# Optimization experiments

Hardware: AMD Instinct MI355X
Metric: run time of the kernel (lower is better)

The kernel has to match this reference:

```python
import jax, jax.numpy as jnp
import numpy as np

N_NODES = 100000
N_EDGES = 3200000
N_GRAPHS = 1000
FEAT = 512
EMB = 7
N_CLASSES = 10


def gcn_conv(x, W, b, src, dst, n_nodes):
    # PyG GCNConv: add self-loops, symmetric normalization, aggregate src->dst.
    h = x @ W  # [N, emb] — transform first (emb is tiny)
    loops = jnp.arange(n_nodes, dtype=src.dtype)
    es = jnp.concatenate([src, loops])
    ed = jnp.concatenate([dst, loops])
    deg = jax.ops.segment_sum(jnp.ones_like(ed, dtype=h.dtype), ed, num_segments=n_nodes)
    dinv = jnp.where(deg > 0, jax.lax.rsqrt(deg), 0.0)
    norm = dinv[es] * dinv[ed]  # [E+N]
    msgs = h[es] * norm[:, None]
    out = jax.ops.segment_sum(msgs, ed, num_segments=n_nodes)
    return out + b


def setup_inputs() -> dict:
    key = jax.random.key(0)
    ks = jax.random.split(key, 8)
    x = jax.random.normal(ks[0], (N_NODES, FEAT), dtype=jnp.float32)
    edge_index = jax.random.randint(ks[1], (2, N_EDGES), 0, N_NODES, dtype=jnp.int64)
    batch_index = jnp.sort(jax.random.randint(ks[2], (N_NODES,), 0, N_GRAPHS, dtype=jnp.int64))
    s_in = 1.0 / np.sqrt(FEAT)
    s_h = 1.0 / np.sqrt(EMB)
    W_in = jax.random.uniform(ks[3], (FEAT, EMB), jnp.float32, -s_in, s_in)
    b_in = jnp.zeros((EMB,), jnp.float32)
    W_conv1 = jax.random.uniform(ks[4], (EMB, EMB), jnp.float32, -s_h, s_h)
    b_conv1 = jnp.zeros((EMB,), jnp.float32)
    W_out = jax.random.uniform(ks[5], (EMB, N_CLASSES), jnp.float32, -s_h, s_h)
    b_out = jax.random.uniform(ks[6], (N_CLASSES,), jnp.float32, -s_h, s_h)
    return {"x": x, "edge_index": edge_index, "batch_index": batch_index,
            "W_in": W_in, "b_in": b_in, "W_conv1": W_conv1, "b_conv1": b_conv1,
            "W_out": W_out, "b_out": b_out}


def reference(x, edge_index, batch_index, W_in, b_in, W_conv1, b_conv1, W_out, b_out):
    src, dst = edge_index[0], edge_index[1]
    out = jax.nn.relu(gcn_conv(x, W_in, b_in, src, dst, N_NODES))  # [N, 7]
    # final_conv_acts (computed by the original but NOT used in the returned logits)
    _final_conv_acts = jax.nn.relu(gcn_conv(out, W_conv1, b_conv1, src, dst, N_NODES))
    # global mean pool over batch_index (on `out`, matching the original forward)
    sums = jax.ops.segment_sum(out, batch_index, num_segments=N_GRAPHS)
    counts = jax.ops.segment_sum(jnp.ones((N_NODES,), out.dtype), batch_index, num_segments=N_GRAPHS)
    pooled = sums / jnp.maximum(counts, 1.0)[:, None]  # [G, 7]
    logits = pooled @ W_out + b_out  # [G, classes]
    return jax.nn.softmax(logits, axis=1)
```

## Files before the change

kernel.cpp:

```cpp
#include <hip/hip_runtime.h>

#define N_NODES   100000
#define N_EDGES   3200000
#define N_GRAPHS  1000
#define FEAT      512
#define EMB       7
#define HP        8
#define N_CLASSES 10

#define BSH       8
#define DMASK     255
#define NBUCK     391
#define TCOLS     392
#define NB_A      512
#define TILE_A    6250
#define NIT       25
#define SEGCAP    9216
#define GSPAN     16
#define MM_SB     295
#define MM_NC     96

__device__ __forceinline__ int load_idx(const void* p, long long i, int is32) {
    if (is32) return ((const int*)p)[i];
    return (int)((const long long*)p)[i];
}

__device__ int edge_is32(const void* p) {
    __shared__ int sflag;
    if (threadIdx.x == 0) sflag = 0;
    __syncthreads();
    const int* w = (const int*)p;
    int any = 0;
    for (int k = threadIdx.x; k < 2048; k += blockDim.x)
        if (w[2 * k + 1] != 0) any = 1;
    if (any) atomicOr(&sflag, 1);
    __syncthreads();
    return sflag;
}

__device__ int batch_is32(const void* p) {
    __shared__ int sflag;
    if (threadIdx.x == 0) sflag = 0;
    __syncthreads();
    const int* w = (const int*)p;
    int any = 0;
    for (int k = 1024 + threadIdx.x; k < 2048; k += blockDim.x)
        if (w[2 * k + 1] != 0) any = 1;
    if (any) atomicOr(&sflag, 1);
    __syncthreads();
    return sflag;
}

__device__ void mm_span(int nbase, const float* __restrict__ x,
                        const float* __restrict__ W, float* __restrict__ h) {
    int n = nbase + (int)threadIdx.x;
    if (n >= N_NODES) return;
    const float4* xr = (const float4*)(x + (size_t)n * FEAT);
    float acc[EMB];
#pragma unroll
    for (int j = 0; j < EMB; ++j) acc[j] = 0.0f;
#pragma unroll 4
    for (int k4 = 0; k4 < FEAT / 4; ++k4) {
        float4 v = xr[k4];
        const float* w = W + k4 * 4 * EMB;
#pragma unroll
        for (int j = 0; j < EMB; ++j) {
            float a = acc[j];
            a = fmaf(v.x, w[0 * EMB + j], a);
            a = fmaf(v.y, w[1 * EMB + j], a);
            a = fmaf(v.z, w[2 * EMB + j], a);
            a = fmaf(v.w, w[3 * EMB + j], a);
            acc[j] = a;
        }
    }
    float4* o = (float4*)(h + (size_t)n * HP);
    o[0] = make_float4(acc[0], acc[1], acc[2], acc[3]);
    o[1] = make_float4(acc[4], acc[5], acc[6], 0.0f);
}

__global__ void k_sortblk(const void* __restrict__ eidx, int* __restrict__ T,
                          int* __restrict__ gpk, const float* __restrict__ x,
                          const float* __restrict__ W, float* __restrict__ h) {
    if (blockIdx.x >= NB_A) { mm_span(((int)blockIdx.x - NB_A) * 256, x, W, h); return; }
    __shared__ int stage[TILE_A];
    __shared__ int bins[NBUCK];
    __shared__ int cur[NBUCK];
    __shared__ int pairv[256];
    __shared__ int wsum[4];
    int is32 = edge_is32(eidx);
    const int b = (int)blockIdx.x, t = (int)threadIdx.x;
    for (int k = t; k < NBUCK; k += 256) bins[k] = 0;
    __syncthreads();
    long long e0 = (long long)b * TILE_A;
    int pk[NIT], bk[NIT];
#pragma unroll
    for (int it = 0; it < NIT; ++it) {
        int i = it * 256 + t;
        if (i < TILE_A) {
            int src = load_idx(eidx, e0 + i, is32);
            int d   = load_idx(eidx, (long long)N_EDGES + e0 + i, is32);
            pk[it] = src | ((d & DMASK) << 17);
            bk[it] = d >> BSH;
            atomicAdd(&bins[bk[it]], 1);
        } else { pk[it] = 0; bk[it] = -1; }
    }
    __syncthreads();
    int c0 = (2 * t     < NBUCK) ? bins[2 * t]     : 0;
    int c1 = (2 * t + 1 < NBUCK) ? bins[2 * t + 1] : 0;
    int pr = c0 + c1;
    int inc = pr;
    for (int o = 1; o < 64; o <<= 1) {
        int u = __shfl_up(inc, o);
        if ((t & 63) >= o) inc += u;
    }
    if ((t & 63) == 63) wsum[t >> 6] = inc;
    pairv[t] = inc;
    __syncthreads();
    int add = 0, wv = t >> 6;
    if (wv >= 1) add += wsum[0];
    if (wv >= 2) add += wsum[1];
    if (wv >= 3) add += wsum[2];
    int excl = inc + add - pr;
    __syncthreads();
    if (2 * t     < NBUCK) { bins[2 * t]     = excl;      cur[2 * t]     = excl; }
    if (2 * t + 1 < NBUCK) { bins[2 * t + 1] = excl + c0; cur[2 * t + 1] = excl + c0; }
    __syncthreads();
    for (int k = t; k < NBUCK; k += 256)
        T[b * TCOLS + k] = b * TILE_A + bins[k];
    if (t == 0) T[b * TCOLS + NBUCK] = (b + 1) * TILE_A;
#pragma unroll
    for (int it = 0; it < NIT; ++it) {
        if (bk[it] >= 0) {
            int slot = atomicAdd(&cur[bk[it]], 1);
            stage[slot] = pk[it];
        }
    }
    __syncthreads();
    for (int i = t; i < TILE_A; i += 256)
        gpk[b * TILE_A + i] = stage[i];
}

__device__ int load_runs(const int* __restrict__ T, int k,
                         int* rstart, int* rst, int* wsum) {
    const int t = (int)threadIdx.x;
    int b0 = 2 * t, b1 = 2 * t + 1;
    int s0 = T[b0 * TCOLS + k], e0 = T[b0 * TCOLS + k + 1];
    int s1 = T[b1 * TCOLS + k], e1 = T[b1 * TCOLS + k + 1];
    rstart[b0] = s0; rstart[b1] = s1;
    int c0 = e0 - s0, c1 = e1 - s1;
    int pr = c0 + c1;
    int inc = pr;
    for (int o = 1; o < 64; o <<= 1) {
        int u = __shfl_up(inc, o);
        if ((t & 63) >= o) inc += u;
    }
    if ((t & 63) == 63) wsum[t >> 6] = inc;
    __syncthreads();
    int add = 0, wv = t >> 6;
    if (wv >= 1) add += wsum[0];
    if (wv >= 2) add += wsum[1];
    if (wv >= 3) add += wsum[2];
    int excl = inc + add - pr;
    rst[b0] = excl;
    rst[b1] = excl + c0;
    if (t == 255) rst[512] = excl + pr;
    __syncthreads();
    return rst[512];
}

__device__ __forceinline__ int run_of(const int* rst, int i) {
    int lo = 0, hi = 512;
    while (lo + 1 < hi) { int m = (lo + hi) >> 1; if (rst[m] <= i) lo = m; else hi = m; }
    return lo;
}

__global__ void k_nodecnt(const int* __restrict__ T, const int* __restrict__ gpk,
                          int* __restrict__ cnt, float* __restrict__ gsum,
                          const float* __restrict__ x, const float* __restrict__ W,
                          float* __restrict__ h) {
    if (blockIdx.x >= NBUCK) { mm_span((MM_SB + (int)blockIdx.x - NBUCK) * 256, x, W, h); return; }
    __shared__ int rstart[512], rst[513], wsum[4];
    __shared__ int bin[256];
    const int k = (int)blockIdx.x, t = (int)threadIdx.x;
    if (k < 32) {
        int idx = k * 256 + t;
        if (idx < N_GRAPHS * 8) gsum[idx] = 0.0f;
    }
    bin[t] = 0;
    int total = load_runs(T, k, rstart, rst, wsum);
    __syncthreads();
    int chunk = (total + 255) >> 8;
    int i0 = t * chunk;
    int i1 = i0 + chunk; if (i1 > total) i1 = total;
    if (i0 < total) {
        int cur = run_of(rst, i0);
        int nxt = rst[cur + 1];
        int addr = rstart[cur] + (i0 - rst[cur]);
        for (int i = i0; i < i1; ++i) {
            while (i >= nxt) { ++cur; addr = rstart[cur] + (i - rst[cur]); nxt = rst[cur + 1]; }
            int p = gpk[addr++];
            atomicAdd(&bin[(p >> 17) & DMASK], 1);
        }
    }
    __syncthreads();
    int node = (k << BSH) + t;
    if (node < N_NODES) cnt[node] = bin[t];
}

__global__ void k_ggather(const int* __restrict__ T, const int* __restrict__ gpk,
                          const int* __restrict__ cnt, const float* __restrict__ h,
                          const float* __restrict__ b_in, const void* __restrict__ batch,
                          float* __restrict__ gsum) {
    __shared__ int stage[SEGCAP];
    __shared__ int rstart[512], rst[513], wsum[4];
    __shared__ int bin[256], loff[256], curs[256], pairv[256];
    __shared__ float gsl[GSPAN][8];
    __shared__ int gmin_s;
    const int k = (int)blockIdx.x, t = (int)threadIdx.x;
    int bis32 = batch_is32(batch);
    if (t == 0) gmin_s = load_idx(batch, (long long)(k << BSH), bis32);
    if (t < GSPAN * 8) ((float*)gsl)[t] = 0.0f;
    int total = load_runs(T, k, rstart, rst, wsum);
    int len = (total > SEGCAP) ? SEGCAP : total;
    {
        int node = (k << BSH) + t;
        bin[t] = (node < N_NODES) ? cnt[node] : 0;
        curs[t] = 0;
    }
    __syncthreads();
    const int gmin = gmin_s;
    {
        int v = bin[t];
        int inc = v;
        for (int o = 1; o < 64; o <<= 1) {
            int u = __shfl_up(inc, o);
            if ((t & 63) >= o) inc += u;
        }
        pairv[t] = inc;
        __syncthreads();
        int add = 0, wv = t >> 6;
        if (wv >= 1) add += pairv[63];
        if (wv >= 2) add += pairv[127];
        if (wv >= 3) add += pairv[191];
        loff[t] = inc + add - v;
    }
    __syncthreads();
    int chunk = (len + 255) >> 8;
    int i0 = t * chunk;
    int i1 = i0 + chunk; if (i1 > len) i1 = len;
    if (i0 < len) {
        int cur = run_of(rst, i0);
        int nxt = rst[cur + 1];
        int addr = rstart[cur] + (i0 - rst[cur]);
        for (int i = i0; i < i1; ++i) {
            while (i >= nxt) { ++cur; addr = rstart[cur] + (i - rst[cur]); nxt = rst[cur + 1]; }
            int p = gpk[addr++];
            int dl = (p >> 17) & DMASK;
            int r = atomicAdd(&curs[dl], 1);
            stage[loff[dl] + r] = p & 0x1FFFF;
        }
    }
    __syncthreads();
    const float4* h4 = (const float4*)h;
    int q = t & 3;
#pragma unroll
    for (int g4 = 0; g4 < 4; ++g4) {
        int nl = (t >> 2) + g4 * 64;
        int node = (k << BSH) + nl;
        if (node < N_NODES) {
            int o = loff[nl], c = bin[nl];
            float acc[EMB];
#pragma unroll
            for (int j = 0; j < EMB; ++j) acc[j] = 0.0f;
            for (int kk = q; kk < c; kk += 4) {
                int s = stage[o + kk];
                float f = rsqrtf((float)cnt[s] + 1.0f);
                float4 a4 = h4[(size_t)s * 2];
                float4 c4 = h4[(size_t)s * 2 + 1];
                acc[0] = fmaf(a4.x, f, acc[0]); acc[1] = fmaf(a4.y, f, acc[1]);
                acc[2] = fmaf(a4.z, f, acc[2]); acc[3] = fmaf(a4.w, f, acc[3]);
                acc[4] = fmaf(c4.x, f, acc[4]); acc[5] = fmaf(c4.y, f, acc[5]);
                acc[6] = fmaf(c4.z, f, acc[6]);
            }
            float di = rsqrtf((float)c + 1.0f);
            if (q == 0) {
                float4 a4 = h4[(size_t)node * 2];
                float4 c4 = h4[(size_t)node * 2 + 1];
                acc[0] = fmaf(a4.x, di, acc[0]); acc[1] = fmaf(a4.y, di, acc[1]);
                acc[2] = fmaf(a4.z, di, acc[2]); acc[3] = fmaf(a4.w, di, acc[3]);
                acc[4] = fmaf(c4.x, di, acc[4]); acc[5] = fmaf(c4.y, di, acc[5]);
                acc[6] = fmaf(c4.z, di, acc[6]);
            }
#pragma unroll
            for (int j = 0; j < EMB; ++j) {
                acc[j] += __shfl_xor(acc[j], 1);
                acc[j] += __shfl_xor(acc[j], 2);
            }
            int j0 = 2 * q;
            float v0 = fmaxf(fmaf(di, acc[j0], b_in[j0]), 0.0f);
            float v1 = (j0 + 1 < EMB)
                     ? fmaxf(fmaf(di, acc[j0 + 1], b_in[j0 + 1]), 0.0f) : 0.0f;
            int g = load_idx(batch, node, bis32);
            int gi = g - gmin;
            if (gi < GSPAN) {
                atomicAdd(&gsl[gi][j0], v0);
                atomicAdd(&gsl[gi][j0 + 1], v1);
            } else {
                atomicAdd(&gsum[(size_t)g * 8 + j0], v0);
                atomicAdd(&gsum[(size_t)g * 8 + j0 + 1], v1);
            }
        }
    }
    __syncthreads();
    if (t < GSPAN * 8) {
        int r = t >> 3, c = t & 7;
        float v = gsl[r][c];
        int g = gmin + r;
        if (v != 0.0f && g < N_GRAPHS) atomicAdd(&gsum[(size_t)g * 8 + c], v);
    }
}

__global__ void k_final(const float* __restrict__ gsum, const void* __restrict__ batch,
                        const float* __restrict__ W_out, const float* __restrict__ b_out,
                        float* __restrict__ out) {
    int is32 = batch_is32(batch);
    int g = (int)blockIdx.x * 256 + (int)threadIdx.x;
    if (g >= N_GRAPHS) return;
    int n0, n1;
    {
        int lo = 0, hi = N_NODES;
        while (lo < hi) { int m = (lo + hi) >> 1; if (load_idx(batch, m, is32) < g) lo = m + 1; else hi = m; }
        n0 = lo;
        hi = N_NODES;
        while (lo < hi) { int m = (lo + hi) >> 1; if (load_idx(batch, m, is32) < g + 1) lo = m + 1; else hi = m; }
        n1 = lo;
    }
    float inv = 1.0f / fmaxf((float)(n1 - n0), 1.0f);
    float sums[EMB];
#pragma unroll
    for (int j = 0; j < EMB; ++j) sums[j] = gsum[(size_t)g * 8 + j] * inv;
    float logit[N_CLASSES];
    float mx = -1e30f;
#pragma unroll
    for (int c = 0; c < N_CLASSES; ++c) {
        float l = b_out[c];
#pragma unroll
        for (int j = 0; j < EMB; ++j)
            l = fmaf(sums[j], W_out[j * N_CLASSES + c], l);
        logit[c] = l;
        mx = fmaxf(mx, l);
    }
    float se = 0.0f;
#pragma unroll
    for (int c = 0; c < N_CLASSES; ++c) {
        logit[c] = expf(logit[c] - mx);
        se += logit[c];
    }
    float is = 1.0f / se;
#pragma unroll
    for (int c = 0; c < N_CLASSES; ++c)
        out[(size_t)g * N_CLASSES + c] = logit[c] * is;
}

extern "C" void kernel_launch(void* const* d_in, const int* in_sizes, int n_in,
                              void* d_out, int out_size, void* d_ws, size_t ws_size,
                              hipStream_t stream) {
    const float* x     = (const float*)d_in[0];
    const void*  eidx  = d_in[1];
    const void*  batch = d_in[2];
    const float* W_in  = (const float*)d_in[3];
    const float* b_in  = (const float*)d_in[4];
    const float* W_out = (const float*)d_in[7];
    const float* b_out = (const float*)d_in[8];
    float* out = (float*)d_out;

    int*   gpk  = (int*)d_ws;
    int*   T    = gpk + N_EDGES;
    int*   cnt  = T + NB_A * TCOLS;
    float* h    = (float*)(cnt + N_NODES);
    float* gsum = h + (size_t)N_NODES * HP;

    const int B = 256;
    k_sortblk<<<NB_A + MM_SB, B, 0, stream>>>(eidx, T, gpk, x, W_in, h);
    k_nodecnt<<<NBUCK + MM_NC, B, 0, stream>>>(T, gpk, cnt, gsum, x, W_in, h);
    k_ggather<<<NBUCK, B, 0, stream>>>(T, gpk, cnt, h, b_in, batch, gsum);
    k_final  <<<(N_GRAPHS + B - 1) / B, B, 0, stream>>>(gsum, batch, W_out, b_out, out);
}
```

Before: 157.8 us.

## Use 512-thread blocks and fold final softmax into last gather block

The count and gather kernels now run with 512 threads per block, so each thread loads one tile's run bounds instead of two and the scans widen to eight waves. The separate final kernel is removed: the last block to finish the gather, found through an atomic done counter with a threadfence, computes the pooled means and softmax. This saves one kernel launch and may raise per-block parallelism. In exchange, the final stage runs serially inside a single block. The mm_span calls inside the count kernel are reindexed with a 512-row stride, so there are now half as many of those blocks.

```diff
diff --git a/kernel.cpp b/kernel.cpp
--- a/kernel.cpp
+++ b/kernel.cpp
@@ -18,7 +18,7 @@
 #define SEGCAP    9216
 #define GSPAN     16
 #define MM_SB     295
-#define MM_NC     96
+#define MM_NC     48
 
 __device__ __forceinline__ int load_idx(const void* p, long long i, int is32) {
     if (is32) return ((const int*)p)[i];
@@ -140,56 +140,45 @@
         gpk[b * TILE_A + i] = stage[i];
 }
 
-__device__ int load_runs(const int* __restrict__ T, int k,
-                         int* rstart, int* rst, int* wsum) {
-    const int t = (int)threadIdx.x;
-    int b0 = 2 * t, b1 = 2 * t + 1;
-    int s0 = T[b0 * TCOLS + k], e0 = T[b0 * TCOLS + k + 1];
-    int s1 = T[b1 * TCOLS + k], e1 = T[b1 * TCOLS + k + 1];
-    rstart[b0] = s0; rstart[b1] = s1;
-    int c0 = e0 - s0, c1 = e1 - s1;
-    int pr = c0 + c1;
-    int inc = pr;
-    for (int o = 1; o < 64; o <<= 1) {
-        int u = __shfl_up(inc, o);
-        if ((t & 63) >= o) inc += u;
-    }
-    if ((t & 63) == 63) wsum[t >> 6] = inc;
-    __syncthreads();
-    int add = 0, wv = t >> 6;
-    if (wv >= 1) add += wsum[0];
-    if (wv >= 2) add += wsum[1];
-    if (wv >= 3) add += wsum[2];
-    int excl = inc + add - pr;
-    rst[b0] = excl;
-    rst[b1] = excl + c0;
-    if (t == 255) rst[512] = excl + pr;
-    __syncthreads();
-    return rst[512];
-}
-
 __device__ __forceinline__ int run_of(const int* rst, int i) {
     int lo = 0, hi = 512;
     while (lo + 1 < hi) { int m = (lo + hi) >> 1; if (rst[m] <= i) lo = m; else hi = m; }
     return lo;
 }
 
-__global__ void k_nodecnt(const int* __restrict__ T, const int* __restrict__ gpk,
-                          int* __restrict__ cnt, float* __restrict__ gsum,
-                          const float* __restrict__ x, const float* __restrict__ W,
-                          float* __restrict__ h) {
-    if (blockIdx.x >= NBUCK) { mm_span((MM_SB + (int)blockIdx.x - NBUCK) * 256, x, W, h); return; }
-    __shared__ int rstart[512], rst[513], wsum[4];
+__global__ void __launch_bounds__(512)
+k_nodecnt(const int* __restrict__ T, const int* __restrict__ gpk,
+          int* __restrict__ cnt, float* __restrict__ gsum, int* __restrict__ done,
+          const float* __restrict__ x, const float* __restrict__ W,
+          float* __restrict__ h) {
+    if (blockIdx.x >= NBUCK) { mm_span(MM_SB * 256 + ((int)blockIdx.x - NBUCK) * 512, x, W, h); return; }
+    __shared__ int rstart[512], rst[513], wsum[8];
     __shared__ int bin[256];
     const int k = (int)blockIdx.x, t = (int)threadIdx.x;
-    if (k < 32) {
-        int idx = k * 256 + t;
+    if (k < 16) {
+        int idx = k * 512 + t;
         if (idx < N_GRAPHS * 8) gsum[idx] = 0.0f;
-    }
-    bin[t] = 0;
-    int total = load_runs(T, k, rstart, rst, wsum);
-    __syncthreads();
-    int chunk = (total + 255) >> 8;
+        if (idx == 0) *done = 0;
+    }
+    if (t < 256) bin[t] = 0;
+    int s = T[t * TCOLS + k], e = T[t * TCOLS + k + 1];
+    rstart[t] = s;
+    int c = e - s;
+    int inc = c;
+    for (int o = 1; o < 64; o <<= 1) {
+        int u = __shfl_up(inc, o);
+        if ((t & 63) >= o) inc += u;
+    }
+    if ((t & 63) == 63) wsum[t >> 6] = inc;
+    __syncthreads();
+    int add = 0, wv = t >> 6;
+#pragma unroll
+    for (int w = 0; w < 8; ++w) if (w < wv) add += wsum[w];
+    rst[t] = inc + add - c;
+    if (t == 511) rst[512] = inc + add;
+    __syncthreads();
+    int total = rst[512];
+    int chunk = (total + 511) >> 9;
     int i0 = t * chunk;
     int i1 = i0 + chunk; if (i1 > total) i1 = total;
     if (i0 < total) {
@@ -204,48 +193,68 @@
     }
     __syncthreads();
     int node = (k << BSH) + t;
-    if (node < N_NODES) cnt[node] = bin[t];
-}
-
-__global__ void k_ggather(const int* __restrict__ T, const int* __restrict__ gpk,
-                          const int* __restrict__ cnt, const float* __restrict__ h,
-                          const float* __restrict__ b_in, const void* __restrict__ batch,
-                          float* __restrict__ gsum) {
+    if (t < 256 && node < N_NODES) cnt[node] = bin[t];
+}
+
+__global__ void __launch_bounds__(512)
+k_ggather(const int* __restrict__ T, const int* __restrict__ gpk,
+          const int* __restrict__ cnt, const float* __restrict__ h,
+          const float* __restrict__ b_in, const void* __restrict__ batch,
+          float* __restrict__ gsum, int* __restrict__ done,
+          const float* __restrict__ W_out, const float* __restrict__ b_out,
+          float* __restrict__ out) {
     __shared__ int stage[SEGCAP];
-    __shared__ int rstart[512], rst[513], wsum[4];
+    __shared__ int rstart[512], rst[513], wsum[8];
     __shared__ int bin[256], loff[256], curs[256], pairv[256];
     __shared__ float gsl[GSPAN][8];
-    __shared__ int gmin_s;
+    __shared__ int gmin_s, lastf;
     const int k = (int)blockIdx.x, t = (int)threadIdx.x;
     int bis32 = batch_is32(batch);
     if (t == 0) gmin_s = load_idx(batch, (long long)(k << BSH), bis32);
     if (t < GSPAN * 8) ((float*)gsl)[t] = 0.0f;
-    int total = load_runs(T, k, rstart, rst, wsum);
-    int len = (total > SEGCAP) ? SEGCAP : total;
-    {
+    if (t < 256) {
         int node = (k << BSH) + t;
         bin[t] = (node < N_NODES) ? cnt[node] : 0;
         curs[t] = 0;
     }
+    int s = T[t * TCOLS + k], e = T[t * TCOLS + k + 1];
+    rstart[t] = s;
+    int c = e - s;
+    int inc = c;
+    for (int o = 1; o < 64; o <<= 1) {
+        int u = __shfl_up(inc, o);
+        if ((t & 63) >= o) inc += u;
+    }
+    if ((t & 63) == 63) wsum[t >> 6] = inc;
     __syncthreads();
     const int gmin = gmin_s;
-    {
+    int add = 0, wv = t >> 6;
+#pragma unroll
+    for (int w = 0; w < 8; ++w) if (w < wv) add += wsum[w];
+    rst[t] = inc + add - c;
+    if (t == 511) rst[512] = inc + add;
+    if (t < 256) {
         int v = bin[t];
-        int inc = v;
+        int inc2 = v;
         for (int o = 1; o < 64; o <<= 1) {
-            int u = __shfl_up(inc, o);
-            if ((t & 63) >= o) inc += u;
-        }
-        pairv[t] = inc;
-        __syncthreads();
-        int add = 0, wv = t >> 6;
-        if (wv >= 1) add += pairv[63];
-        if (wv >= 2) add += pairv[127];
-        if (wv >= 3) add += pairv[191];
-        loff[t] = inc + add - v;
-    }
-    __syncthreads();
-    int chunk = (len + 255) >> 8;
+            int u = __shfl_up(inc2, o);
+            if ((t & 63) >= o) inc2 += u;
+        }
+        pairv[t] = inc2;
+    }
+    __syncthreads();
+    if (t < 256) {
+        int v = bin[t];
+        int add2 = 0, w2 = t >> 6;
+        if (w2 >= 1) add2 += pairv[63];
+        if (w2 >= 2) add2 += pairv[127];
+        if (w2 >= 3) add2 += pairv[191];
+        loff[t] = pairv[t] + add2 - v;
+    }
+    __syncthreads();
+    int total = rst[512];
+    int len = (total > SEGCAP) ? SEGCAP : total;
+    int chunk = (len + 511) >> 9;
     int i0 = t * chunk;
     int i1 = i0 + chunk; if (i1 > len) i1 = len;
     if (i0 < len) {
@@ -264,25 +273,25 @@
     const float4* h4 = (const float4*)h;
     int q = t & 3;
 #pragma unroll
-    for (int g4 = 0; g4 < 4; ++g4) {
-        int nl = (t >> 2) + g4 * 64;
+    for (int g4 = 0; g4 < 2; ++g4) {
+        int nl = (t >> 2) + g4 * 128;
         int node = (k << BSH) + nl;
         if (node < N_NODES) {
-            int o = loff[nl], c = bin[nl];
+            int o = loff[nl], cc = bin[nl];
             float acc[EMB];
 #pragma unroll
             for (int j = 0; j < EMB; ++j) acc[j] = 0.0f;
-            for (int kk = q; kk < c; kk += 4) {
-                int s = stage[o + kk];
-                float f = rsqrtf((float)cnt[s] + 1.0f);
-                float4 a4 = h4[(size_t)s * 2];
-                float4 c4 = h4[(size_t)s * 2 + 1];
+            for (int kk = q; kk < cc; kk += 4) {
+                int sn = stage[o + kk];
+                float f = rsqrtf((float)cnt[sn] + 1.0f);
+                float4 a4 = h4[(size_t)sn * 2];
+                float4 c4 = h4[(size_t)sn * 2 + 1];
                 acc[0] = fmaf(a4.x, f, acc[0]); acc[1] = fmaf(a4.y, f, acc[1]);
                 acc[2] = fmaf(a4.z, f, acc[2]); acc[3] = fmaf(a4.w, f, acc[3]);
                 acc[4] = fmaf(c4.x, f, acc[4]); acc[5] = fmaf(c4.y, f, acc[5]);
                 acc[6] = fmaf(c4.z, f, acc[6]);
             }
-            float di = rsqrtf((float)c + 1.0f);
+            float di = rsqrtf((float)cc + 1.0f);
             if (q == 0) {
                 float4 a4 = h4[(size_t)node * 2];
                 float4 c4 = h4[(size_t)node * 2 + 1];
@@ -313,53 +322,57 @@
     }
     __syncthreads();
     if (t < GSPAN * 8) {
-        int r = t >> 3, c = t & 7;
-        float v = gsl[r][c];
+        int r = t >> 3, cc = t & 7;
+        float v = gsl[r][cc];
         int g = gmin + r;
-        if (v != 0.0f && g < N_GRAPHS) atomicAdd(&gsum[(size_t)g * 8 + c], v);
-    }
-}
-
-__global__ void k_final(const float* __restrict__ gsum, const void* __restrict__ batch,
-                        const float* __restrict__ W_out, const float* __restrict__ b_out,
-                        float* __restrict__ out) {
-    int is32 = batch_is32(batch);
-    int g = (int)blockIdx.x * 256 + (int)threadIdx.x;
-    if (g >= N_GRAPHS) return;
-    int n0, n1;
-    {
-        int lo = 0, hi = N_NODES;
-        while (lo < hi) { int m = (lo + hi) >> 1; if (load_idx(batch, m, is32) < g) lo = m + 1; else hi = m; }
-        n0 = lo;
-        hi = N_NODES;
-        while (lo < hi) { int m = (lo + hi) >> 1; if (load_idx(batch, m, is32) < g + 1) lo = m + 1; else hi = m; }
-        n1 = lo;
-    }
-    float inv = 1.0f / fmaxf((float)(n1 - n0), 1.0f);
-    float sums[EMB];
-#pragma unroll
-    for (int j = 0; j < EMB; ++j) sums[j] = gsum[(size_t)g * 8 + j] * inv;
-    float logit[N_CLASSES];
-    float mx = -1e30f;
-#pragma unroll
-    for (int c = 0; c < N_CLASSES; ++c) {
-        float l = b_out[c];
-#pragma unroll
-        for (int j = 0; j < EMB; ++j)
-            l = fmaf(sums[j], W_out[j * N_CLASSES + c], l);
-        logit[c] = l;
-        mx = fmaxf(mx, l);
-    }
-    float se = 0.0f;
-#pragma unroll
-    for (int c = 0; c < N_CLASSES; ++c) {
-        logit[c] = expf(logit[c] - mx);
-        se += logit[c];
-    }
-    float is = 1.0f / se;
-#pragma unroll
-    for (int c = 0; c < N_CLASSES; ++c)
-        out[(size_t)g * N_CLASSES + c] = logit[c] * is;
+        if (v != 0.0f && g < N_GRAPHS) atomicAdd(&gsum[(size_t)g * 8 + cc], v);
+    }
+    __syncthreads();
+    if (t == 0) {
+        __threadfence();
+        int prev = atomicAdd(done, 1);
+        lastf = (prev == NBUCK - 1) ? 1 : 0;
+    }
+    __syncthreads();
+    if (lastf) {
+        for (int g = t; g < N_GRAPHS; g += 512) {
+            int n0, n1;
+            {
+                int lo = 0, hi = N_NODES;
+                while (lo < hi) { int m = (lo + hi) >> 1; if (load_idx(batch, m, bis32) < g) lo = m + 1; else hi = m; }
+                n0 = lo;
+                hi = N_NODES;
+                while (lo < hi) { int m = (lo + hi) >> 1; if (load_idx(batch, m, bis32) < g + 1) lo = m + 1; else hi = m; }
+                n1 = lo;
+            }
+            float inv = 1.0f / fmaxf((float)(n1 - n0), 1.0f);
+            float sums[EMB];
+#pragma unroll
+            for (int j = 0; j < EMB; ++j)
+                sums[j] = atomicAdd(&gsum[(size_t)g * 8 + j], 0.0f) * inv;
+            float logit[N_CLASSES];
+            float mx = -1e30f;
+#pragma unroll
+            for (int cc = 0; cc < N_CLASSES; ++cc) {
+                float l = b_out[cc];
+#pragma unroll
+                for (int j = 0; j < EMB; ++j)
+                    l = fmaf(sums[j], W_out[j * N_CLASSES + cc], l);
+                logit[cc] = l;
+                mx = fmaxf(mx, l);
+            }
+            float se = 0.0f;
+#pragma unroll
+            for (int cc = 0; cc < N_CLASSES; ++cc) {
+                logit[cc] = expf(logit[cc] - mx);
+                se += logit[cc];
+            }
+            float is = 1.0f / se;
+#pragma unroll
+            for (int cc = 0; cc < N_CLASSES; ++cc)
+                out[(size_t)g * N_CLASSES + cc] = logit[cc] * is;
+        }
+    }
 }
 
 extern "C" void kernel_launch(void* const* d_in, const int* in_sizes, int n_in,
@@ -379,10 +392,11 @@
     int*   cnt  = T + NB_A * TCOLS;
     float* h    = (float*)(cnt + N_NODES);
     float* gsum = h + (size_t)N_NODES * HP;
+    int*   done = (int*)(gsum + N_GRAPHS * 8);
 
     const int B = 256;
     k_sortblk<<<NB_A + MM_SB, B, 0, stream>>>(eidx, T, gpk, x, W_in, h);
-    k_nodecnt<<<NBUCK + MM_NC, B, 0, stream>>>(T, gpk, cnt, gsum, x, W_in, h);
-    k_ggather<<<NBUCK, B, 0, stream>>>(T, gpk, cnt, h, b_in, batch, gsum);
-    k_final  <<<(N_GRAPHS + B - 1) / B, B, 0, stream>>>(gsum, batch, W_out, b_out, out);
-}
+    k_nodecnt<<<NBUCK + MM_NC, 512, 0, stream>>>(T, gpk, cnt, gsum, done, x, W_in, h);
+    k_ggather<<<NBUCK, 512, 0, stream>>>(T, gpk, cnt, h, b_in, batch, gsum, done,
+                                         W_out, b_out, out);
+}
```

New measurement: 189.1 us. +19.8%, slower.

## Prescale h by source degree norm in nodecnt, move full matmul to sortblk

Applied to the files above, without the earlier changes.

The per-node x@W projection now runs entirely in k_sortblk's extra blocks, so k_nodecnt no longer does a share of it. k_nodecnt then multiplies each node's h row by its own rsqrt degree factor right after computing counts. The gather loop can then sum neighbour rows directly, without loading cnt[s] per edge and computing an rsqrt, which removes a random 4-byte load per edge. The cost is one extra read-modify-write pass over h, and the whole matmul now sits in the first kernel.

```diff
diff --git a/kernel.cpp b/kernel.cpp
--- a/kernel.cpp
+++ b/kernel.cpp
@@ -17,8 +17,7 @@
 #define NIT       25
 #define SEGCAP    9216
 #define GSPAN     16
-#define MM_SB     295
-#define MM_NC     96
+#define MMF       391
 
 __device__ __forceinline__ int load_idx(const void* p, long long i, int is32) {
     if (is32) return ((const int*)p)[i];
@@ -176,9 +175,7 @@
 
 __global__ void k_nodecnt(const int* __restrict__ T, const int* __restrict__ gpk,
                           int* __restrict__ cnt, float* __restrict__ gsum,
-                          const float* __restrict__ x, const float* __restrict__ W,
                           float* __restrict__ h) {
-    if (blockIdx.x >= NBUCK) { mm_span((MM_SB + (int)blockIdx.x - NBUCK) * 256, x, W, h); return; }
     __shared__ int rstart[512], rst[513], wsum[4];
     __shared__ int bin[256];
     const int k = (int)blockIdx.x, t = (int)threadIdx.x;
@@ -204,7 +201,15 @@
     }
     __syncthreads();
     int node = (k << BSH) + t;
-    if (node < N_NODES) cnt[node] = bin[t];
+    if (node < N_NODES) {
+        int c = bin[t];
+        cnt[node] = c;
+        float di = rsqrtf((float)c + 1.0f);
+        float4* hp = (float4*)(h + (size_t)node * HP);
+        float4 a = hp[0], cc = hp[1];
+        hp[0] = make_float4(a.x * di, a.y * di, a.z * di, a.w * di);
+        hp[1] = make_float4(cc.x * di, cc.y * di, cc.z * di, 0.0f);
+    }
 }
 
 __global__ void k_ggather(const int* __restrict__ T, const int* __restrict__ gpk,
@@ -274,28 +279,23 @@
             for (int j = 0; j < EMB; ++j) acc[j] = 0.0f;
             for (int kk = q; kk < c; kk += 4) {
                 int s = stage[o + kk];
-                float f = rsqrtf((float)cnt[s] + 1.0f);
                 float4 a4 = h4[(size_t)s * 2];
                 float4 c4 = h4[(size_t)s * 2 + 1];
-                acc[0] = fmaf(a4.x, f, acc[0]); acc[1] = fmaf(a4.y, f, acc[1]);
-                acc[2] = fmaf(a4.z, f, acc[2]); acc[3] = fmaf(a4.w, f, acc[3]);
-                acc[4] = fmaf(c4.x, f, acc[4]); acc[5] = fmaf(c4.y, f, acc[5]);
-                acc[6] = fmaf(c4.z, f, acc[6]);
+                acc[0] += a4.x; acc[1] += a4.y; acc[2] += a4.z; acc[3] += a4.w;
+                acc[4] += c4.x; acc[5] += c4.y; acc[6] += c4.z;
             }
-            float di = rsqrtf((float)c + 1.0f);
             if (q == 0) {
                 float4 a4 = h4[(size_t)node * 2];
                 float4 c4 = h4[(size_t)node * 2 + 1];
-                acc[0] = fmaf(a4.x, di, acc[0]); acc[1] = fmaf(a4.y, di, acc[1]);
-                acc[2] = fmaf(a4.z, di, acc[2]); acc[3] = fmaf(a4.w, di, acc[3]);
-                acc[4] = fmaf(c4.x, di, acc[4]); acc[5] = fmaf(c4.y, di, acc[5]);
-                acc[6] = fmaf(c4.z, di, acc[6]);
+                acc[0] += a4.x; acc[1] += a4.y; acc[2] += a4.z; acc[3] += a4.w;
+                acc[4] += c4.x; acc[5] += c4.y; acc[6] += c4.z;
             }
 #pragma unroll
             for (int j = 0; j < EMB; ++j) {
                 acc[j] += __shfl_xor(acc[j], 1);
                 acc[j] += __shfl_xor(acc[j], 2);
             }
+            float di = rsqrtf((float)c + 1.0f);
             int j0 = 2 * q;
             float v0 = fmaxf(fmaf(di, acc[j0], b_in[j0]), 0.0f);
             float v1 = (j0 + 1 < EMB)
@@ -381,8 +381,8 @@
     float* gsum = h + (size_t)N_NODES * HP;
 
     const int B = 256;
-    k_sortblk<<<NB_A + MM_SB, B, 0, stream>>>(eidx, T, gpk, x, W_in, h);
-    k_nodecnt<<<NBUCK + MM_NC, B, 0, stream>>>(T, gpk, cnt, gsum, x, W_in, h);
+    k_sortblk<<<NB_A + MMF, B, 0, stream>>>(eidx, T, gpk, x, W_in, h);
+    k_nodecnt<<<NBUCK, B, 0, stream>>>(T, gpk, cnt, gsum, h);
     k_ggather<<<NBUCK, B, 0, stream>>>(T, gpk, cnt, h, b_in, batch, gsum);
     k_final  <<<(N_GRAPHS + B - 1) / B, B, 0, stream>>>(gsum, batch, W_out, b_out, out);
 }
```

After: 135.6 us (median of 2 runs). 1.16x faster.
